# Kernel optimization log

Measured on AMD Instinct MI355X. Metric: run time of the kernel, lower is better.

## Reference

```python
import jax, jax.numpy as jnp
import numpy as np

BN_EPS = 1e-5
K = 3  # k_size


def _unfold(x, k):
    # torch F.unfold with padding=k//2, stride=1, viewed as (B, C, k*k, H, W).
    # Kernel positions are row-major (i slow, j fast), matching torch layout.
    p = k // 2
    B, C, H, W = x.shape
    xp = jnp.pad(x, ((0, 0), (0, 0), (p, p), (p, p)))
    pats = jnp.stack([xp[:, :, i:i + H, j:j + W]
                      for i in range(k) for j in range(k)], axis=2)
    return pats  # (B, C, k*k, H, W)


def _conv1x1(x, w, b):
    # w: (C_out, C_in), x: (B, C_in, H, W)
    return jnp.einsum('oc,bchw->bohw', w, x) + b[None, :, None, None]


def _bn(x, gamma, beta, mean, var):
    inv = gamma / jnp.sqrt(var + BN_EPS)
    return x * inv[None, :, None, None] + (beta - mean * inv)[None, :, None, None]


def setup_inputs() -> dict:
    key = jax.random.key(0)
    ks = jax.random.split(key, 12)
    B, C, H, W = 8, 256, 64, 64
    s = lambda k_, *sh: jax.random.normal(k_, sh, dtype=jnp.float32) * 0.05
    return {
        'x': jax.random.normal(ks[0], (B, C, H, W), dtype=jnp.float32),
        # feature_embedding: Conv2d(C, C, 1) + BN
        'w_embed': s(ks[1], C, C), 'b_embed': jnp.zeros((C,), jnp.float32),
        'bn1_gamma': jnp.ones((C,), jnp.float32), 'bn1_beta': jnp.zeros((C,), jnp.float32),
        'bn1_mean': jnp.zeros((C,), jnp.float32), 'bn1_var': jnp.ones((C,), jnp.float32),
        # enhance: Conv2d(2C, C, 1) + BN
        'w_enh': s(ks[2], C, 2 * C), 'b_enh': jnp.zeros((C,), jnp.float32),
        'bn2_gamma': jnp.ones((C,), jnp.float32), 'bn2_beta': jnp.zeros((C,), jnp.float32),
        'bn2_mean': jnp.zeros((C,), jnp.float32), 'bn2_var': jnp.ones((C,), jnp.float32),
        # weight_gen: Conv2d(2C, C//4, 1) -> ReLU -> Conv2d(C//4, C, 1) -> Sigmoid
        'w_g1': s(ks[3], C // 4, 2 * C), 'b_g1': jnp.zeros((C // 4,), jnp.float32),
        'w_g2': s(ks[4], C, C // 4), 'b_g2': jnp.zeros((C,), jnp.float32),
    }


def reference(x, w_embed, b_embed, bn1_gamma, bn1_beta, bn1_mean, bn1_var,
              w_enh, b_enh, bn2_gamma, bn2_beta, bn2_mean, bn2_var,
              w_g1, b_g1, w_g2, b_g2):
    B, C, H, W = x.shape
    # ---- feature embedding: 1x1 conv + BN (eval) + ReLU
    fe = jax.nn.relu(_bn(_conv1x1(x, w_embed, b_embed),
                         bn1_gamma, bn1_beta, bn1_mean, bn1_var))
    # ---- region similarity: cosine(center pixel, each kxk neighbor) over C
    pats = _unfold(fe, K)                       # (B, C, k2, H, W)
    sim = jnp.einsum('bchw,bckhw->bkhw', fe, pats)
    norm_c = jnp.sqrt(jnp.sum(fe * fe, axis=1))             # (B, H, W)
    norm_p = jnp.sqrt(jnp.sum(pats * pats, axis=1))         # (B, k2, H, W)
    sim = sim / (norm_c[:, None] * norm_p + 1e-7)
    sim = jax.nn.softmax(sim, axis=1)                       # over k2 window
    # ---- dynamic feature aggregation on original x
    xpats = _unfold(x, K)                                   # (B, C, k2, H, W)
    agg = jnp.einsum('bckhw,bkhw->bchw', xpats, sim)
    enhanced = jax.nn.relu(_bn(_conv1x1(jnp.concatenate([x, agg], axis=1), w_enh, b_enh),
                               bn2_gamma, bn2_beta, bn2_mean, bn2_var))
    # ---- output modulation (SE-style gating)
    pooled = jnp.mean(jnp.concatenate([x, enhanced], axis=1), axis=(2, 3), keepdims=True)
    h = jax.nn.relu(_conv1x1(pooled, w_g1, b_g1))
    weights = jax.nn.sigmoid(_conv1x1(h, w_g2, b_g2))       # (B, C, 1, 1)
    return x + weights * enhanced
```

## Files before the change

### kernel.cpp

```cpp
#include <hip/hip_runtime.h>
#include <math.h>

typedef unsigned short u16;
typedef unsigned int   u32;
typedef __attribute__((ext_vector_type(8))) short short8;
typedef __attribute__((ext_vector_type(4))) short s16x4;
typedef __attribute__((ext_vector_type(4))) float f32x4;

#define OFS_XB   0ul
#define OFS_W1B  8388608ul
#define OFS_W2B  8421376ul
#define OFS_B1   8486912ul
#define OFS_B2   8487168ul
#define OFS_POOL 8487424ul
#define OFS_ENH  8491520ul
#define OFS_XC   16880128ul

__device__ __forceinline__ u16 f2bf(float x) {
    union { float f; u32 u; } v; v.f = x;
    u32 r = v.u + 0x7fffu + ((v.u >> 16) & 1u);
    return (u16)(r >> 16);
}
__device__ __forceinline__ float bf2f(u16 h) {
    union { u32 u; float f; } v; v.u = ((u32)h) << 16;
    return v.f;
}
__device__ __forceinline__ void ld_g2l_16(u16* l, const u16* g) {
    __builtin_amdgcn_global_load_lds(
        (const __attribute__((address_space(1))) u32*)g,
        (__attribute__((address_space(3))) u32*)l,
        16, 0, 0);
}

__global__ __launch_bounds__(256) void k_cvt(
    const float* __restrict__ x, u16* __restrict__ xb, u16* __restrict__ xc,
    float* __restrict__ pool,
    const float* __restrict__ w1, const float* __restrict__ b1,
    const float* __restrict__ g1, const float* __restrict__ be1,
    const float* __restrict__ m1, const float* __restrict__ v1,
    const float* __restrict__ w2, const float* __restrict__ b2,
    const float* __restrict__ g2, const float* __restrict__ be2,
    const float* __restrict__ m2, const float* __restrict__ v2,
    u16* __restrict__ w1b, u16* __restrict__ w2b,
    float* __restrict__ b1f, float* __restrict__ b2f)
{
    __shared__ float tile[64][65];
    const int t = threadIdx.x;
    const int id = blockIdx.x;
    if (id < 1) {
        const float4 z = {0.f, 0.f, 0.f, 0.f};
#pragma unroll
        for (int i = 0; i < 4; ++i) ((float4*)pool)[i * 256 + t] = z;
        return;
    }
    if (id < 771) {
        int idx = (id - 1) * 256 + t;
        if (idx < 65536) {
            int o = idx >> 8;
            float inv = g1[o] * rsqrtf(v1[o] + 1e-5f);
            w1b[idx] = f2bf(w1[idx] * inv);
        } else if (idx < 196608) {
            int j = idx - 65536;
            int o = j >> 9;
            float inv = g2[o] * rsqrtf(v2[o] + 1e-5f);
            w2b[j] = f2bf(w2[j] * inv);
        } else if (idx < 196864) {
            int o = idx - 196608;
            float inv = g1[o] * rsqrtf(v1[o] + 1e-5f);
            b1f[o] = b1[o] * inv + be1[o] - m1[o] * inv;
        } else if (idx < 197120) {
            int o = idx - 196864;
            float inv = g2[o] * rsqrtf(v2[o] + 1e-5f);
            b2f[o] = b2[o] * inv + be2[o] - m2[o] * inv;
        }
        return;
    }
    const int cid = id - 771;
    const int pt = cid & 63, ct = (cid >> 6) & 3, b = cid >> 8;
    const float* src = x + (((size_t)(b * 256 + ct * 64)) << 12) + pt * 64;
#pragma unroll
    for (int i = 0; i < 16; ++i) {
        int idx = i * 256 + t;
        int cl = idx >> 6, pl = idx & 63;
        tile[cl][pl] = src[((size_t)cl << 12) + pl];
    }
    __syncthreads();
#pragma unroll
    for (int i = 0; i < 8; ++i) {
        int idx = i * 256 + t;
        int pl = idx >> 5, c2 = idx & 31;
        int cl = c2 * 2;
        u32 lo = f2bf(tile[cl][pl]);
        u32 hi = f2bf(tile[cl + 1][pl]);
        *(u32*)(xb + (((size_t)(b * 4096 + pt * 64 + pl)) << 9) + ct * 64 + cl) = lo | (hi << 16);
    }
#pragma unroll
    for (int i = 0; i < 8; ++i) {
        int idx = i * 256 + t;
        int cl = idx >> 5, pl2 = (idx & 31) * 2;
        u32 lo = f2bf(tile[cl][pl2]);
        u32 hi = f2bf(tile[cl][pl2 + 1]);
        *(u32*)(xc + (((size_t)(b * 256 + ct * 64 + cl)) << 12) + pt * 64 + pl2) = lo | (hi << 16);
    }
    if (t < 64) {
        float s = 0.f;
#pragma unroll
        for (int i = 0; i < 64; ++i) s += tile[t][i];
        atomicAdd(&pool[(b << 9) + ct * 64 + t], s * (1.f / 4096.f));
    }
}

template<int KIN, bool OUTT, bool DOPOOL>
__global__ __launch_bounds__(256) void k_gemm(
    const u16* __restrict__ xb, const u16* __restrict__ Wb,
    const float* __restrict__ biasf, void* __restrict__ outp,
    float* __restrict__ poolp)
{
    __shared__ __align__(16) u16 Wl[4096];
    __shared__ __align__(16) u16 Xl[4096];
    __shared__ __align__(16) u16 ct[OUTT ? 16384 : 4];
    __shared__ float sbias[128];
    const int t = threadIdx.x;
    const int lane = t & 63;
    const int wv = t >> 6;
    const int id = blockIdx.x;
    const int p_blk = (((id >> 4) << 3) | (id & 7)) * 128;
    const int o_blk = ((id >> 3) & 1) * 128;
    const int owg = (wv & 1) * 4;
    const int pwg = (wv >> 1) * 4;
    const int r16 = lane & 15, q = lane >> 4;
    if (t < 128) sbias[t] = biasf[o_blk + t];

    f32x4 acc[4][4];
#pragma unroll
    for (int i = 0; i < 4; ++i)
#pragma unroll
        for (int j = 0; j < 4; ++j) acc[i][j] = (f32x4){0.f, 0.f, 0.f, 0.f};

    for (int kc = 0; kc < KIN / 32; ++kc) {
        const int kk = kc * 32 + q * 8;
#pragma unroll
        for (int s = 0; s < 4; ++s) {
            const int bi = wv * 4 + s;
            const u16* g;
            u16* l;
            if (bi < 8) {
                g = Wb + (size_t)(o_blk + bi * 16 + r16) * KIN + kk;
                l = Wl + bi * 512;
            } else {
                g = xb + (((size_t)(p_blk + (bi - 8) * 16 + r16)) << 9) + kk;
                l = Xl + (bi - 8) * 512;
            }
            ld_g2l_16(l, g);
        }
        __syncthreads();
        short8 af[4], bf[4];
#pragma unroll
        for (int i = 0; i < 4; ++i) af[i] = *(const short8*)(Wl + (owg + i) * 512 + lane * 8);
#pragma unroll
        for (int j = 0; j < 4; ++j) bf[j] = *(const short8*)(Xl + (pwg + j) * 512 + lane * 8);
#pragma unroll
        for (int i = 0; i < 4; ++i)
#pragma unroll
            for (int j = 0; j < 4; ++j)
                acc[i][j] = __builtin_amdgcn_mfma_f32_16x16x32_bf16(af[i], bf[j], acc[i][j], 0, 0, 0);
        __syncthreads();
    }

    float bia[4][4];
#pragma unroll
    for (int i = 0; i < 4; ++i)
#pragma unroll
        for (int r = 0; r < 4; ++r) bia[i][r] = sbias[owg * 16 + i * 16 + q * 4 + r];
    const int bidx = p_blk >> 12;

    if (OUTT) {
#pragma unroll
        for (int i = 0; i < 4; ++i) {
#pragma unroll
            for (int j = 0; j < 4; ++j) {
                const int px_l = pwg * 16 + j * 16 + r16;
#pragma unroll
                for (int rp = 0; rp < 2; ++rp) {
                    const int r0 = rp * 2;
                    const int o_l = owg * 16 + i * 16 + q * 4 + r0;
                    const float v0 = fmaxf(acc[i][j][r0] + bia[i][r0], 0.f);
                    const float v1 = fmaxf(acc[i][j][r0 + 1] + bia[i][r0 + 1], 0.f);
                    const u32 pk = (u32)f2bf(v0) | ((u32)f2bf(v1) << 16);
                    *(u32*)((char*)ct + px_l * 256 + ((o_l * 2) ^ ((px_l & 7) << 4))) = pk;
                }
            }
        }
        __syncthreads();
        u16* feT = (u16*)outp;
#pragma unroll
        for (int it = 0; it < 16; ++it) {
            const int idx = it * 256 + t;
            const int px_l = idx >> 5, cd = idx & 31;
            s16x4 v = *(const s16x4*)((char*)ct + px_l * 256 + ((cd * 8) ^ ((px_l & 7) << 4)));
            *(s16x4*)(feT + (((size_t)(bidx * 4096 + (p_blk & 4095) + px_l)) << 8) + o_blk + cd * 4) = v;
        }
        return;
    }

    const int pin0 = (p_blk & 4095) + pwg * 16 + r16;
#pragma unroll
    for (int i = 0; i < 4; ++i) {
#pragma unroll
        for (int r = 0; r < 4; ++r) {
            const int o = o_blk + owg * 16 + i * 16 + q * 4 + r;
            const size_t rowb = ((size_t)(bidx * 256 + o)) << 12;
            float ps = 0.f;
#pragma unroll
            for (int j = 0; j < 4; ++j) {
                float v = fmaxf(acc[i][j][r] + bia[i][r], 0.f);
                const size_t oi = rowb + pin0 + j * 16;
                ((u16*)outp)[oi] = f2bf(v);
                ps += v;
            }
            if (DOPOOL) {
                ps += __shfl_down(ps, 8, 16);
                ps += __shfl_down(ps, 4, 16);
                ps += __shfl_down(ps, 2, 16);
                ps += __shfl_down(ps, 1, 16);
                if (r16 == 0)
                    atomicAdd(&poolp[(bidx << 9) + 256 + o], ps * (1.f / 4096.f));
            }
        }
    }
}

__global__ __launch_bounds__(512) void k_simagg(
    const u16* __restrict__ fe, const u16* __restrict__ xb, u16* __restrict__ xbo)
{
    __shared__ float red[8][65][13];
    __shared__ float ws9[9][64];
    const int t = threadIdx.x;
    const int id = blockIdx.x;
    const int b = id & 7, h = id >> 3;
    const int rows[3] = {h > 0 ? h - 1 : 0, h, h < 63 ? h + 1 : 63};

    {
        const int px = t >> 3, c8 = t & 7;
        const int pxl = px > 0 ? px - 1 : 0, pxr = px < 63 ? px + 1 : 63;
        const int pxs[3] = {pxl, px, pxr};
        const u16* feb = fe + (((size_t)(b * 4096)) << 8) + c8 * 8;
        float cvec[32];
        float dot[9];
        float nn0 = 0.f, nn2 = 0.f;
        {
            const u16* p = feb + (((size_t)(rows[1] * 64 + px)) << 8);
            float s = 0.f;
#pragma unroll
            for (int i = 0; i < 4; ++i) {
                short8 v = *(const short8*)(p + i * 64);
#pragma unroll
                for (int u = 0; u < 8; ++u) {
                    float f = bf2f((u16)v[u]);
                    cvec[i * 8 + u] = f;
                    s = fmaf(f, f, s);
                }
            }
            dot[4] = s;
        }
#pragma unroll
        for (int r = 0; r < 3; ++r) {
#pragma unroll
            for (int j = 0; j < 3; ++j) {
                if (r == 1 && j == 1) continue;
                const int k = r * 3 + j;
                const u16* p = feb + (((size_t)(rows[r] * 64 + pxs[j])) << 8);
                float s = 0.f, qq = 0.f;
#pragma unroll
                for (int i = 0; i < 4; ++i) {
                    short8 v = *(const short8*)(p + i * 64);
#pragma unroll
                    for (int u = 0; u < 8; ++u) {
                        float f = bf2f((u16)v[u]);
                        s = fmaf(cvec[i * 8 + u], f, s);
                        if (j == 1) qq = fmaf(f, f, qq);
                    }
                }
                dot[k] = s;
                if (j == 1) { if (r == 0) nn0 = qq; else nn2 = qq; }
            }
        }
#pragma unroll
        for (int k = 0; k < 9; ++k) red[c8][px][k] = dot[k];
        red[c8][px][9] = nn0;
        red[c8][px][10] = nn2;
    }
    __syncthreads();
    if (t < 64) {
        const int w = t;
        float dk[9];
#pragma unroll
        for (int k = 0; k < 9; ++k) {
            float s = red[0][w][k];
#pragma unroll
            for (int g = 1; g < 8; ++g) s += red[g][w][k];
            dk[k] = s;
        }
        float nr0 = red[0][w][9], nr2 = red[0][w][10];
#pragma unroll
        for (int g = 1; g < 8; ++g) { nr0 += red[g][w][9]; nr2 += red[g][w][10]; }
        float nr[3] = {nr0, dk[4], nr2};
        const float nc = sqrtf(dk[4]);
        float sv[9], mk[9];
#pragma unroll
        for (int di = -1; di <= 1; ++di) {
#pragma unroll
            for (int dj = -1; dj <= 1; ++dj) {
                const int k = (di + 1) * 3 + (dj + 1);
                const int hn = h + di, wn = w + dj;
                const float mask = (hn >= 0 && hn < 64 && wn >= 0 && wn < 64) ? 1.f : 0.f;
                const int wc = wn < 0 ? 0 : (wn > 63 ? 63 : wn);
                const float nk = __shfl(nr[di + 1], wc, 64);
                mk[k] = mask;
                sv[k] = mask * dk[k] / (nc * sqrtf(nk) + 1e-7f);
            }
        }
        float mx = sv[0];
#pragma unroll
        for (int k = 1; k < 9; ++k) mx = fmaxf(mx, sv[k]);
        float e[9], sum = 0.f;
#pragma unroll
        for (int k = 0; k < 9; ++k) { e[k] = expf(sv[k] - mx); sum += e[k]; }
        const float rs = 1.f / sum;
#pragma unroll
        for (int k = 0; k < 9; ++k) ws9[k][w] = mk[k] * e[k] * rs;
    }
    __syncthreads();
    const int cd = t & 63, pxg = t >> 6;
    const u16* xbb = xb + (((size_t)(b * 4096)) << 9) + cd * 4;
    u16* orow = xbo + (((size_t)(b * 4096 + h * 64)) << 9) + 256 + cd * 4;
#pragma unroll
    for (int pi = 0; pi < 8; ++pi) {
        const int px = pxg * 8 + pi;
        const int pL = px > 0 ? px - 1 : 0, pR = px < 63 ? px + 1 : 63;
        const int pxs2[3] = {pL, px, pR};
        float m9[9];
#pragma unroll
        for (int k = 0; k < 9; ++k) m9[k] = ws9[k][px];
        float a0 = 0.f, a1 = 0.f, a2 = 0.f, a3 = 0.f;
#pragma unroll
        for (int r = 0; r < 3; ++r) {
#pragma unroll
            for (int j = 0; j < 3; ++j) {
                const float m = m9[r * 3 + j];
                s16x4 v = *(const s16x4*)(xbb + (((size_t)(rows[r] * 64 + pxs2[j])) << 9));
                a0 = fmaf(bf2f((u16)v[0]), m, a0);
                a1 = fmaf(bf2f((u16)v[1]), m, a1);
                a2 = fmaf(bf2f((u16)v[2]), m, a2);
                a3 = fmaf(bf2f((u16)v[3]), m, a3);
            }
        }
        s16x4 sv4;
        sv4[0] = (short)f2bf(a0); sv4[1] = (short)f2bf(a1);
        sv4[2] = (short)f2bf(a2); sv4[3] = (short)f2bf(a3);
        *(s16x4*)(orow + ((size_t)px << 9)) = sv4;
    }
}

__global__ __launch_bounds__(256) void k_final(
    const u16* __restrict__ xc, const u16* __restrict__ enh,
    const float* __restrict__ pool,
    const float* __restrict__ wg1, const float* __restrict__ bg1,
    const float* __restrict__ wg2, const float* __restrict__ bg2,
    float* __restrict__ out)
{
    __shared__ float pl[512];
    __shared__ float hpart[4][64];
    __shared__ float hb[64];
    __shared__ float sg[256];
    const int t = threadIdx.x;
    const int id = blockIdx.x;
    const int b = id & 7, cg = id >> 3;
    pl[t] = pool[b * 512 + t];
    pl[t + 256] = pool[b * 512 + 256 + t];
    __syncthreads();
    {
        const int o = t & 63, seg = t >> 6;
        float s = 0.f;
        const float* wr_ = wg1 + o * 512 + seg * 128;
        const float* pr_ = pl + seg * 128;
#pragma unroll 4
        for (int j = 0; j < 128; ++j) s = fmaf(wr_[j], pr_[j], s);
        hpart[seg][o] = s;
    }
    __syncthreads();
    if (t < 64)
        hb[t] = fmaxf(hpart[0][t] + hpart[1][t] + hpart[2][t] + hpart[3][t] + bg1[t], 0.f);
    __syncthreads();
    {
        float s2 = bg2[t];
        const float* w2 = wg2 + t * 64;
#pragma unroll 4
        for (int j = 0; j < 64; ++j) s2 = fmaf(w2[j], hb[j], s2);
        sg[t] = 1.f / (1.f + expf(-s2));
    }
    __syncthreads();
    const int cl = t >> 6, l = t & 63;
    const int c = cg * 4 + cl;
    const float gt = sg[c];
    const u16* xp = xc + (((size_t)(b * 256 + c)) << 12);
    const u16* ep = enh + (((size_t)(b * 256 + c)) << 12);
    float*     op = out + (((size_t)(b * 256 + c)) << 12);
#pragma unroll
    for (int ch = 0; ch < 8; ++ch) {
        const int base = ch * 512 + l * 8;
        short8 ev = *(const short8*)(ep + base);
        short8 xv = *(const short8*)(xp + base);
        float4 o0, o1;
        o0.x = fmaf(gt, bf2f((u16)ev[0]), bf2f((u16)xv[0]));
        o0.y = fmaf(gt, bf2f((u16)ev[1]), bf2f((u16)xv[1]));
        o0.z = fmaf(gt, bf2f((u16)ev[2]), bf2f((u16)xv[2]));
        o0.w = fmaf(gt, bf2f((u16)ev[3]), bf2f((u16)xv[3]));
        o1.x = fmaf(gt, bf2f((u16)ev[4]), bf2f((u16)xv[4]));
        o1.y = fmaf(gt, bf2f((u16)ev[5]), bf2f((u16)xv[5]));
        o1.z = fmaf(gt, bf2f((u16)ev[6]), bf2f((u16)xv[6]));
        o1.w = fmaf(gt, bf2f((u16)ev[7]), bf2f((u16)xv[7]));
        *(float4*)(op + base) = o0;
        *(float4*)(op + base + 4) = o1;
    }
}

extern "C" void kernel_launch(void* const* d_in, const int* in_sizes, int n_in,
                              void* d_out, int out_size, void* d_ws, size_t ws_size,
                              hipStream_t stream)
{
    const float* x       = (const float*)d_in[0];
    const float* w_embed = (const float*)d_in[1];
    const float* b_embed = (const float*)d_in[2];
    const float* g1      = (const float*)d_in[3];
    const float* be1     = (const float*)d_in[4];
    const float* m1      = (const float*)d_in[5];
    const float* v1      = (const float*)d_in[6];
    const float* w_enh   = (const float*)d_in[7];
    const float* b_enh   = (const float*)d_in[8];
    const float* g2      = (const float*)d_in[9];
    const float* be2     = (const float*)d_in[10];
    const float* m2      = (const float*)d_in[11];
    const float* v2      = (const float*)d_in[12];
    const float* w_g1    = (const float*)d_in[13];
    const float* b_g1    = (const float*)d_in[14];
    const float* w_g2    = (const float*)d_in[15];
    const float* b_g2    = (const float*)d_in[16];
    float* ws  = (float*)d_ws;
    float* out = (float*)d_out;

    u16*   xb   = (u16*)(ws + OFS_XB);
    u16*   w1b  = (u16*)(ws + OFS_W1B);
    u16*   w2b  = (u16*)(ws + OFS_W2B);
    float* b1f  = ws + OFS_B1;
    float* b2f  = ws + OFS_B2;
    float* pool = ws + OFS_POOL;
    u16*   enh  = (u16*)(ws + OFS_ENH);
    u16*   xc   = (u16*)(ws + OFS_XC);
    u16*   fe   = (u16*)d_out;

    k_cvt<<<dim3(2819), dim3(256), 0, stream>>>(
        x, xb, xc, pool,
        w_embed, b_embed, g1, be1, m1, v1,
        w_enh, b_enh, g2, be2, m2, v2, w1b, w2b, b1f, b2f);
    k_gemm<256, true, false><<<dim3(512), dim3(256), 0, stream>>>(xb, w1b, b1f, (void*)fe, nullptr);
    k_simagg<<<dim3(512), dim3(512), 0, stream>>>(fe, xb, xb);
    k_gemm<512, false, true><<<dim3(512), dim3(256), 0, stream>>>(xb, w2b, b2f, (void*)enh, pool);
    k_final<<<dim3(512), dim3(256), 0, stream>>>(xc, enh, pool, w_g1, b_g1, w_g2, b_g2, out);
}
```

Baseline: 199.9 us.

## Split similarity-aggregation kernel into 16-pixel row segments with halo norms

Each k_simagg block now handles a 16-pixel segment of a row instead of a whole 64-pixel row. Work is spread over 2048 blocks of 256 threads, with 16 channel slices per pixel. Neighbour norms at the segment edges are computed as halo loads, and the cross-lane shuffle is replaced by a shared-memory lookup. The goal is better occupancy and latency hiding on the small kernel, at the cost of recomputing the halo norms and adding an extra synchronisation.

```diff
diff --git a/kernel.cpp b/kernel.cpp
--- a/kernel.cpp
+++ b/kernel.cpp
@@ -230,36 +230,39 @@
     }
 }
 
-__global__ __launch_bounds__(512) void k_simagg(
+__global__ __launch_bounds__(256) void k_simagg(
     const u16* __restrict__ fe, const u16* __restrict__ xb, u16* __restrict__ xbo)
 {
-    __shared__ float red[8][65][13];
-    __shared__ float ws9[9][64];
+    __shared__ float red[16][17][13];
+    __shared__ float redh[2][3][16];
+    __shared__ float redsum[11][16];
+    __shared__ float nrmh[2][3];
+    __shared__ float ws9[9][16];
     const int t = threadIdx.x;
     const int id = blockIdx.x;
-    const int b = id & 7, h = id >> 3;
+    const int b = id & 7, h = (id >> 3) & 63, q = id >> 9;
+    const int px0 = q * 16;
     const int rows[3] = {h > 0 ? h - 1 : 0, h, h < 63 ? h + 1 : 63};
 
     {
-        const int px = t >> 3, c8 = t & 7;
-        const int pxl = px > 0 ? px - 1 : 0, pxr = px < 63 ? px + 1 : 63;
-        const int pxs[3] = {pxl, px, pxr};
-        const u16* feb = fe + (((size_t)(b * 4096)) << 8) + c8 * 8;
-        float cvec[32];
+        const int pxl = t >> 4, cs = t & 15;
+        const int px = px0 + pxl;
+        const int pxL = px > 0 ? px - 1 : 0, pxR = px < 63 ? px + 1 : 63;
+        const int pxs[3] = {pxL, px, pxR};
+        const u16* feb = fe + (((size_t)(b * 4096)) << 8) + cs * 8;
+        float cvec[16];
         float dot[9];
         float nn0 = 0.f, nn2 = 0.f;
         {
             const u16* p = feb + (((size_t)(rows[1] * 64 + px)) << 8);
+            short8 v0 = *(const short8*)p;
+            short8 v1 = *(const short8*)(p + 128);
             float s = 0.f;
 #pragma unroll
-            for (int i = 0; i < 4; ++i) {
-                short8 v = *(const short8*)(p + i * 64);
-#pragma unroll
-                for (int u = 0; u < 8; ++u) {
-                    float f = bf2f((u16)v[u]);
-                    cvec[i * 8 + u] = f;
-                    s = fmaf(f, f, s);
-                }
+            for (int u = 0; u < 8; ++u) {
+                float f0 = bf2f((u16)v0[u]), f1 = bf2f((u16)v1[u]);
+                cvec[u] = f0; cvec[8 + u] = f1;
+                s = fmaf(f0, f0, s); s = fmaf(f1, f1, s);
             }
             dot[4] = s;
         }
@@ -270,42 +273,58 @@
                 if (r == 1 && j == 1) continue;
                 const int k = r * 3 + j;
                 const u16* p = feb + (((size_t)(rows[r] * 64 + pxs[j])) << 8);
+                short8 v0 = *(const short8*)p;
+                short8 v1 = *(const short8*)(p + 128);
                 float s = 0.f, qq = 0.f;
 #pragma unroll
-                for (int i = 0; i < 4; ++i) {
-                    short8 v = *(const short8*)(p + i * 64);
-#pragma unroll
-                    for (int u = 0; u < 8; ++u) {
-                        float f = bf2f((u16)v[u]);
-                        s = fmaf(cvec[i * 8 + u], f, s);
-                        if (j == 1) qq = fmaf(f, f, qq);
-                    }
+                for (int u = 0; u < 8; ++u) {
+                    float f0 = bf2f((u16)v0[u]), f1 = bf2f((u16)v1[u]);
+                    s = fmaf(cvec[u], f0, s);
+                    s = fmaf(cvec[8 + u], f1, s);
+                    if (j == 1) { qq = fmaf(f0, f0, qq); qq = fmaf(f1, f1, qq); }
                 }
                 dot[k] = s;
                 if (j == 1) { if (r == 0) nn0 = qq; else nn2 = qq; }
             }
         }
 #pragma unroll
-        for (int k = 0; k < 9; ++k) red[c8][px][k] = dot[k];
-        red[c8][px][9] = nn0;
-        red[c8][px][10] = nn2;
-    }
-    __syncthreads();
-    if (t < 64) {
-        const int w = t;
-        float dk[9];
-#pragma unroll
-        for (int k = 0; k < 9; ++k) {
-            float s = red[0][w][k];
-#pragma unroll
-            for (int g = 1; g < 8; ++g) s += red[g][w][k];
-            dk[k] = s;
-        }
-        float nr0 = red[0][w][9], nr2 = red[0][w][10];
-#pragma unroll
-        for (int g = 1; g < 8; ++g) { nr0 += red[g][w][9]; nr2 += red[g][w][10]; }
-        float nr[3] = {nr0, dk[4], nr2};
-        const float nc = sqrtf(dk[4]);
+        for (int k = 0; k < 9; ++k) red[cs][pxl][k] = dot[k];
+        red[cs][pxl][9] = nn0;
+        red[cs][pxl][10] = nn2;
+    }
+    if (t < 96) {
+        const int side = t / 48, rr = (t % 48) / 16, cs = t & 15;
+        const int pxh = side ? (px0 + 16 < 64 ? px0 + 16 : 63) : (px0 > 0 ? px0 - 1 : 0);
+        const u16* p = fe + (((size_t)(b * 4096 + rows[rr] * 64 + pxh)) << 8) + cs * 8;
+        short8 v0 = *(const short8*)p;
+        short8 v1 = *(const short8*)(p + 128);
+        float qq = 0.f;
+#pragma unroll
+        for (int u = 0; u < 8; ++u) {
+            float f0 = bf2f((u16)v0[u]), f1 = bf2f((u16)v1[u]);
+            qq = fmaf(f0, f0, qq); qq = fmaf(f1, f1, qq);
+        }
+        redh[side][rr][cs] = qq;
+    }
+    __syncthreads();
+    if (t < 176) {
+        const int pxl = t & 15, k = t >> 4;
+        float s = 0.f;
+#pragma unroll
+        for (int g = 0; g < 16; ++g) s += red[g][pxl][k];
+        redsum[k][pxl] = s;
+    } else if (t < 182) {
+        const int u_ = t - 176;
+        const int side = u_ / 3, rr = u_ % 3;
+        float s = 0.f;
+#pragma unroll
+        for (int g = 0; g < 16; ++g) s += redh[side][rr][g];
+        nrmh[side][rr] = s;
+    }
+    __syncthreads();
+    if (t < 16) {
+        const int w = px0 + t;
+        const float nc = sqrtf(redsum[4][t]);
         float sv[9], mk[9];
 #pragma unroll
         for (int di = -1; di <= 1; ++di) {
@@ -314,10 +333,15 @@
                 const int k = (di + 1) * 3 + (dj + 1);
                 const int hn = h + di, wn = w + dj;
                 const float mask = (hn >= 0 && hn < 64 && wn >= 0 && wn < 64) ? 1.f : 0.f;
-                const int wc = wn < 0 ? 0 : (wn > 63 ? 63 : wn);
-                const float nk = __shfl(nr[di + 1], wc, 64);
+                const int j = t + dj;
+                const int ridx = di + 1;
+                float nk;
+                if (j < 0)        nk = nrmh[0][ridx];
+                else if (j > 15)  nk = nrmh[1][ridx];
+                else              nk = (ridx == 0) ? redsum[9][j]
+                                     : (ridx == 1) ? redsum[4][j] : redsum[10][j];
                 mk[k] = mask;
-                sv[k] = mask * dk[k] / (nc * sqrtf(nk) + 1e-7f);
+                sv[k] = mask * redsum[k][t] / (nc * sqrtf(nk) + 1e-7f);
             }
         }
         float mx = sv[0];
@@ -328,20 +352,21 @@
         for (int k = 0; k < 9; ++k) { e[k] = expf(sv[k] - mx); sum += e[k]; }
         const float rs = 1.f / sum;
 #pragma unroll
-        for (int k = 0; k < 9; ++k) ws9[k][w] = mk[k] * e[k] * rs;
-    }
-    __syncthreads();
-    const int cd = t & 63, pxg = t >> 6;
+        for (int k = 0; k < 9; ++k) ws9[k][t] = mk[k] * e[k] * rs;
+    }
+    __syncthreads();
+    const int cd = t & 63, pg = t >> 6;
     const u16* xbb = xb + (((size_t)(b * 4096)) << 9) + cd * 4;
     u16* orow = xbo + (((size_t)(b * 4096 + h * 64)) << 9) + 256 + cd * 4;
 #pragma unroll
-    for (int pi = 0; pi < 8; ++pi) {
-        const int px = pxg * 8 + pi;
+    for (int pi = 0; pi < 4; ++pi) {
+        const int pxl = pg * 4 + pi;
+        const int px = px0 + pxl;
         const int pL = px > 0 ? px - 1 : 0, pR = px < 63 ? px + 1 : 63;
         const int pxs2[3] = {pL, px, pR};
         float m9[9];
 #pragma unroll
-        for (int k = 0; k < 9; ++k) m9[k] = ws9[k][px];
+        for (int k = 0; k < 9; ++k) m9[k] = ws9[k][pxl];
         float a0 = 0.f, a1 = 0.f, a2 = 0.f, a3 = 0.f;
 #pragma unroll
         for (int r = 0; r < 3; ++r) {
@@ -464,7 +489,7 @@
         w_embed, b_embed, g1, be1, m1, v1,
         w_enh, b_enh, g2, be2, m2, v2, w1b, w2b, b1f, b2f);
     k_gemm<256, true, false><<<dim3(512), dim3(256), 0, stream>>>(xb, w1b, b1f, (void*)fe, nullptr);
-    k_simagg<<<dim3(512), dim3(512), 0, stream>>>(fe, xb, xb);
+    k_simagg<<<dim3(2048), dim3(256), 0, stream>>>(fe, xb, xb);
     k_gemm<512, false, true><<<dim3(512), dim3(256), 0, stream>>>(xb, w2b, b2f, (void*)enh, pool);
     k_final<<<dim3(512), dim3(256), 0, stream>>>(xc, enh, pool, w_g1, b_g1, w_g2, b_g2, out);
 }
```

New measurement: 201.4 us. Within noise of the previous version (+0.7%).
